# Optimization experiments

Hardware: AMD Instinct MI355X
Metric: run time of the kernel (lower is better)

Reference implementation:

```python
import jax, jax.numpy as jnp
import numpy as np

N_CLASSES = 2
N_FEATURES = 10
PSI_DIM = 10


def setup_inputs() -> dict:
    key = jax.random.key(0)
    k1, k2, k3, k4, k5 = jax.random.split(key, 5)
    T = 4_000_000
    x = jax.random.normal(k1, (T, N_FEATURES), dtype=jnp.float32)
    psi_real = jax.random.normal(k2, (PSI_DIM,), dtype=jnp.float32)
    psi_imag = jax.random.normal(k3, (PSI_DIM,), dtype=jnp.float32)
    A_real = jax.random.normal(k4, (N_CLASSES, PSI_DIM, PSI_DIM, N_FEATURES), dtype=jnp.float32)
    A_imag = jax.random.normal(k5, (N_CLASSES, PSI_DIM, PSI_DIM, N_FEATURES), dtype=jnp.float32)
    return {"x": x, "psi_real": psi_real, "psi_imag": psi_imag,
            "A_real": A_real, "A_imag": A_imag}


def _mat(psi1, A, psi2):
    # Batch-independent contraction of the 'i' and 'j' axes: [k, a]
    return jnp.einsum('i,kija,j->ka', psi1, A, psi2)


def reference(x, psi_real, psi_imag, A_real, A_imag):
    x_real = x
    x_imag = jnp.zeros_like(x)
    # Sign pattern from the original 8-term sum:
    #   +rRr -rIr(xi) -iRr(xi) -iIr(xr) -rRi(xr) +rIi(xi) +iRi(xi) +iIi(xr)
    # Coefficient matrix multiplying x_real:
    M_r = (_mat(psi_real, A_real, psi_real)
           - _mat(psi_imag, A_imag, psi_real)
           - _mat(psi_real, A_real, psi_imag)
           + _mat(psi_imag, A_imag, psi_imag))  # [k, a]
    # Coefficient matrix multiplying x_imag:
    M_i = (-_mat(psi_real, A_imag, psi_real)
           - _mat(psi_imag, A_real, psi_real)
           + _mat(psi_real, A_imag, psi_imag)
           + _mat(psi_imag, A_real, psi_imag))  # [k, a]
    # result[t, k] = sum_a x[t, a] * M[k, a]
    return x_real @ M_r.T + x_imag @ M_i.T
```

## Files before the change

kernel.cpp:

```cpp
#include <hip/hip_runtime.h>

constexpr int NC = 2;
constexpr int NF = 10;
constexpr int PD = 10;

constexpr int THREADS = 256;
constexpr int F4_PER_THREAD = 5;
constexpr int TILE_F4 = THREADS * F4_PER_THREAD;
constexpr int TILE_FLOATS = TILE_F4 * 4;

__global__ __launch_bounds__(THREADS) void fused_complexnet_kernel(
        const float* __restrict__ x,
        const float* __restrict__ psi_r,
        const float* __restrict__ psi_i,
        const float* __restrict__ A_r,
        const float* __restrict__ A_i,
        float* __restrict__ out,
        int T2, long totalF4) {
    __shared__ float Msh[NC * NF];
    __shared__ float part[NC * NF * PD];
    __shared__ float tile[TILE_FLOATS];

    const int t = threadIdx.x;

    if (t < NC * NF * PD) {
        int k = t / (NF * PD);
        int rem = t - k * (NF * PD);
        int a = rem / PD;
        int i = rem - a * PD;
        float pri = psi_r[i], pii = psi_i[i];
        float acc = 0.f;
#pragma unroll
        for (int j = 0; j < PD; ++j) {
            float dj = psi_r[j] - psi_i[j];
            int idx = ((k * PD + i) * PD + j) * NF + a;
            acc = fmaf(pri * A_r[idx] - pii * A_i[idx], dj, acc);
        }
        part[t] = acc;
    }
    __syncthreads();
    if (t < NC * NF) {
        int k = t / NF, a = t - k * NF;
        float s = 0.f;
#pragma unroll
        for (int i = 0; i < PD; ++i) s += part[(k * NF + a) * PD + i];
        Msh[t] = s;
    }
    __syncthreads();

    float m0[NF], m1[NF];
#pragma unroll
    for (int a = 0; a < NF; ++a) {
        m0[a] = Msh[a];
        m1[a] = Msh[NF + a];
    }

    const float4* x4 = reinterpret_cast<const float4*>(x);
    float4* out4 = reinterpret_cast<float4*>(out);
    const int nTiles = (T2 + THREADS - 1) / THREADS;
    const int waveBaseF = (t & ~63) * 4;

    for (int tileIdx = blockIdx.x; tileIdx < nTiles; tileIdx += (int)gridDim.x) {
        const long base4 = (long)tileIdx * TILE_F4;
#pragma unroll
        for (int q = 0; q < F4_PER_THREAD; ++q) {
            long g4 = base4 + (long)q * THREADS + t;
            if (g4 >= totalF4) g4 = totalF4 - 1;
            const float* ldsdst = &tile[q * (THREADS * 4) + waveBaseF];
            __builtin_amdgcn_global_load_lds(
                (const __attribute__((address_space(1))) void*)(x4 + g4),
                (__attribute__((address_space(3))) void*)ldsdst,
                16, 0, 0);
        }
        __syncthreads();

        const int rp = tileIdx * THREADS + t;
        if (rp < T2) {
            const float4* lp = reinterpret_cast<const float4*>(&tile[t * 20]);
            float4 v0 = lp[0], v1 = lp[1], v2 = lp[2], v3 = lp[3], v4 = lp[4];
            float r0[NF] = {v0.x, v0.y, v0.z, v0.w, v1.x, v1.y, v1.z, v1.w, v2.x, v2.y};
            float r1[NF] = {v2.z, v2.w, v3.x, v3.y, v3.z, v3.w, v4.x, v4.y, v4.z, v4.w};
            float4 o = {0.f, 0.f, 0.f, 0.f};
#pragma unroll
            for (int a = 0; a < NF; ++a) {
                o.x = fmaf(r0[a], m0[a], o.x);
                o.y = fmaf(r0[a], m1[a], o.y);
                o.z = fmaf(r1[a], m0[a], o.z);
                o.w = fmaf(r1[a], m1[a], o.w);
            }
            out4[rp] = o;
        }
        __syncthreads();
    }
}

extern "C" void kernel_launch(void* const* d_in, const int* in_sizes, int n_in,
                              void* d_out, int out_size, void* d_ws, size_t ws_size,
                              hipStream_t stream) {
    const float* x     = (const float*)d_in[0];
    const float* psi_r = (const float*)d_in[1];
    const float* psi_i = (const float*)d_in[2];
    const float* A_r   = (const float*)d_in[3];
    const float* A_i   = (const float*)d_in[4];
    float* out = (float*)d_out;

    const int T = in_sizes[0] / NF;
    const int T2 = T / 2;
    const long totalF4 = (long)in_sizes[0] / 4;

    const int nTiles = (T2 + THREADS - 1) / THREADS;
    int blocks = nTiles < 1792 ? nTiles : 1792;

    fused_complexnet_kernel<<<blocks, THREADS, 0, stream>>>(
        x, psi_r, psi_i, A_r, A_i, out, T2, totalF4);
}
```

Baseline: 34.34 us.

## Double-buffer LDS tile loads with single-wave blocks and vmcnt waits

Switches to 64-thread single-wave blocks, so the per-tile __syncthreads barriers can be replaced by explicit s_waitcnt vmcnt counting. Adds a second LDS buffer so the next tile's global_load_lds is issued before the current tile is computed. The M coefficient reduction is collapsed into one 20-thread loop, and the grid grows to 3584 blocks. The vmcnt counts assume the output stores and staging loads are counted exactly as predicted, which risks a data race if the compiler schedules them differently. Each block also repeats a longer serial M setup.

```diff
diff --git a/kernel.cpp b/kernel.cpp
--- a/kernel.cpp
+++ b/kernel.cpp
@@ -4,47 +4,38 @@
 constexpr int NF = 10;
 constexpr int PD = 10;
 
-constexpr int THREADS = 256;
+constexpr int THREADS = 64;
 constexpr int F4_PER_THREAD = 5;
 constexpr int TILE_F4 = THREADS * F4_PER_THREAD;
 constexpr int TILE_FLOATS = TILE_F4 * 4;
 
-__global__ __launch_bounds__(THREADS) void fused_complexnet_kernel(
+__global__ __launch_bounds__(THREADS) void fused_dbuf_kernel(
         const float* __restrict__ x,
         const float* __restrict__ psi_r,
         const float* __restrict__ psi_i,
         const float* __restrict__ A_r,
         const float* __restrict__ A_i,
         float* __restrict__ out,
-        int T2, long totalF4) {
+        int T2, long totalF4, int nTiles) {
     __shared__ float Msh[NC * NF];
-    __shared__ float part[NC * NF * PD];
-    __shared__ float tile[TILE_FLOATS];
+    __shared__ float tile[2][TILE_FLOATS];
 
     const int t = threadIdx.x;
 
-    if (t < NC * NF * PD) {
-        int k = t / (NF * PD);
-        int rem = t - k * (NF * PD);
-        int a = rem / PD;
-        int i = rem - a * PD;
-        float pri = psi_r[i], pii = psi_i[i];
+    if (t < NC * NF) {
+        int k = t / NF, a = t - k * NF;
         float acc = 0.f;
 #pragma unroll
-        for (int j = 0; j < PD; ++j) {
-            float dj = psi_r[j] - psi_i[j];
-            int idx = ((k * PD + i) * PD + j) * NF + a;
-            acc = fmaf(pri * A_r[idx] - pii * A_i[idx], dj, acc);
+        for (int i = 0; i < PD; ++i) {
+            float pri = psi_r[i], pii = psi_i[i];
+#pragma unroll
+            for (int j = 0; j < PD; ++j) {
+                float dj = psi_r[j] - psi_i[j];
+                int idx = ((k * PD + i) * PD + j) * NF + a;
+                acc = fmaf(pri * A_r[idx] - pii * A_i[idx], dj, acc);
+            }
         }
-        part[t] = acc;
-    }
-    __syncthreads();
-    if (t < NC * NF) {
-        int k = t / NF, a = t - k * NF;
-        float s = 0.f;
-#pragma unroll
-        for (int i = 0; i < PD; ++i) s += part[(k * NF + a) * PD + i];
-        Msh[t] = s;
+        Msh[t] = acc;
     }
     __syncthreads();
 
@@ -57,40 +48,55 @@
 
     const float4* x4 = reinterpret_cast<const float4*>(x);
     float4* out4 = reinterpret_cast<float4*>(out);
-    const int nTiles = (T2 + THREADS - 1) / THREADS;
-    const int waveBaseF = (t & ~63) * 4;
+    const int G = (int)gridDim.x;
 
-    for (int tileIdx = blockIdx.x; tileIdx < nTiles; tileIdx += (int)gridDim.x) {
+    auto STAGE = [&](int buf, int tileIdx) {
         const long base4 = (long)tileIdx * TILE_F4;
 #pragma unroll
         for (int q = 0; q < F4_PER_THREAD; ++q) {
             long g4 = base4 + (long)q * THREADS + t;
             if (g4 >= totalF4) g4 = totalF4 - 1;
-            const float* ldsdst = &tile[q * (THREADS * 4) + waveBaseF];
+            const float* ldsdst = &tile[buf][q * (THREADS * 4)];
             __builtin_amdgcn_global_load_lds(
                 (const __attribute__((address_space(1))) void*)(x4 + g4),
                 (__attribute__((address_space(3))) void*)ldsdst,
                 16, 0, 0);
         }
-        __syncthreads();
+    };
 
-        const int rp = tileIdx * THREADS + t;
-        if (rp < T2) {
-            const float4* lp = reinterpret_cast<const float4*>(&tile[t * 20]);
-            float4 v0 = lp[0], v1 = lp[1], v2 = lp[2], v3 = lp[3], v4 = lp[4];
-            float r0[NF] = {v0.x, v0.y, v0.z, v0.w, v1.x, v1.y, v1.z, v1.w, v2.x, v2.y};
-            float r1[NF] = {v2.z, v2.w, v3.x, v3.y, v3.z, v3.w, v4.x, v4.y, v4.z, v4.w};
-            float4 o = {0.f, 0.f, 0.f, 0.f};
+    int cur = 0;
+    const int firstTile = (int)blockIdx.x;
+    if (firstTile < nTiles) STAGE(0, firstTile);
+
+    int iter = 0;
+    for (int k = firstTile; k < nTiles; k += G, ++iter) {
+        const int next = k + G;
+        const bool hasNext = next < nTiles;
+        if (hasNext) STAGE(cur ^ 1, next);
+
+        const int n = (hasNext ? 5 : 0) + (iter ? 1 : 0);
+        if (n == 6)      asm volatile("s_waitcnt vmcnt(6)" ::: "memory");
+        else if (n == 5) asm volatile("s_waitcnt vmcnt(5)" ::: "memory");
+        else if (n == 1) asm volatile("s_waitcnt vmcnt(1)" ::: "memory");
+        else             asm volatile("s_waitcnt vmcnt(0)" ::: "memory");
+
+        const int rp = k * THREADS + t;
+        const float4* lp = reinterpret_cast<const float4*>(&tile[cur][t * 20]);
+        float4 v0 = lp[0], v1 = lp[1], v2 = lp[2], v3 = lp[3], v4 = lp[4];
+        float r0[NF] = {v0.x, v0.y, v0.z, v0.w, v1.x, v1.y, v1.z, v1.w, v2.x, v2.y};
+        float r1[NF] = {v2.z, v2.w, v3.x, v3.y, v3.z, v3.w, v4.x, v4.y, v4.z, v4.w};
+        float4 o = {0.f, 0.f, 0.f, 0.f};
 #pragma unroll
-            for (int a = 0; a < NF; ++a) {
-                o.x = fmaf(r0[a], m0[a], o.x);
-                o.y = fmaf(r0[a], m1[a], o.y);
-                o.z = fmaf(r1[a], m0[a], o.z);
-                o.w = fmaf(r1[a], m1[a], o.w);
-            }
-            out4[rp] = o;
+        for (int a = 0; a < NF; ++a) {
+            o.x = fmaf(r0[a], m0[a], o.x);
+            o.y = fmaf(r0[a], m1[a], o.y);
+            o.z = fmaf(r1[a], m0[a], o.z);
+            o.w = fmaf(r1[a], m1[a], o.w);
         }
-        __syncthreads();
+        if (rp < T2) out4[rp] = o;
+
+        asm volatile("" ::: "memory");
+        cur ^= 1;
     }
 }
 
@@ -107,10 +113,11 @@
     const int T = in_sizes[0] / NF;
     const int T2 = T / 2;
     const long totalF4 = (long)in_sizes[0] / 4;
+    const int nTiles = (T2 + THREADS - 1) / THREADS;
 
-    const int nTiles = (T2 + THREADS - 1) / THREADS;
-    int blocks = nTiles < 1792 ? nTiles : 1792;
+    int blocks = 14 * 256;
+    if (blocks > nTiles) blocks = nTiles;
 
-    fused_complexnet_kernel<<<blocks, THREADS, 0, stream>>>(
-        x, psi_r, psi_i, A_r, A_i, out, T2, totalF4);
+    fused_dbuf_kernel<<<blocks, THREADS, 0, stream>>>(
+        x, psi_r, psi_i, A_r, A_i, out, T2, totalF4, nTiles);
 }
```

Result: slower. 36.68 us (+6.8%).
